# Optimization experiments

Hardware: AMD Instinct MI355X
Metric: run time of the kernel (lower is better)

Reference implementation:

```python
import jax, jax.numpy as jnp
import numpy as np

B, T, C = 2, 2048, 1024
N_HEAD = 16
HEAD_DIM = C // N_HEAD


def setup_inputs() -> dict:
    key = jax.random.key(0)
    k1, k2, k3 = jax.random.split(key, 3)
    x = jax.random.normal(k1, (B, T, C), dtype=jnp.float32)
    w_qkv = jax.random.normal(k2, (C, 3 * C), dtype=jnp.float32) * (C ** -0.5)
    w_proj = jax.random.normal(k3, (C, C), dtype=jnp.float32) * (C ** -0.5)
    b_proj = jnp.zeros((C,), dtype=jnp.float32)
    return {"x": x, "w_qkv": w_qkv, "w_proj": w_proj, "b_proj": b_proj}


def reference(x, w_qkv, w_proj, b_proj):
    Bx, Tx, Cx = x.shape
    # qkv projection: [B,T,3C] -> split into q,k,v each [B,H,T,D]
    qkv = x @ w_qkv  # [B,T,3C]
    qkv = qkv.reshape(Bx, Tx, 3, N_HEAD, HEAD_DIM)
    q = qkv[:, :, 0].transpose(0, 2, 1, 3)  # [B,H,T,D]
    k = qkv[:, :, 1].transpose(0, 2, 1, 3)
    v = qkv[:, :, 2].transpose(0, 2, 1, 3)
    scale = 1.0 / np.sqrt(HEAD_DIM).astype(np.float32)
    att = jnp.einsum('bhtd,bhsd->bhts', q, k) * scale  # [B,H,T,T]
    causal = jnp.tril(jnp.ones((Tx, Tx), dtype=bool))
    att = jnp.where(causal[None, None], att, -jnp.inf)
    att = jax.nn.softmax(att, axis=-1)
    # dropout p=0.0 -> identity (eval-mode math)
    y = jnp.einsum('bhts,bhsd->bhtd', att, v)  # [B,H,T,D]
    y = y.transpose(0, 2, 1, 3).reshape(Bx, Tx, Cx)
    return y @ w_proj + b_proj
```

## Files before the change

### kernel.cpp

```cpp
#include <hip/hip_runtime.h>

typedef __bf16 bf16x8 __attribute__((ext_vector_type(8)));
typedef float f32x4 __attribute__((ext_vector_type(4)));
typedef unsigned short u16;
typedef unsigned int u32;
typedef u32 u32x4 __attribute__((ext_vector_type(4)));
typedef u16 u16x8 __attribute__((ext_vector_type(8)));

#define B_ 2
#define T_ 2048
#define C_ 1024
#define H_ 16
#define D_ 64
#define QSCALE 0.18033688011112042f

__device__ __forceinline__ u16 f2bf(float f) {
    u32 u = __builtin_bit_cast(u32, f);
    u += 0x7fffu + ((u >> 16) & 1u);
    return (u16)(u >> 16);
}

__device__ __forceinline__ f32x4 mfma16(bf16x8 a, bf16x8 b, f32x4 c) {
    return __builtin_amdgcn_mfma_f32_16x16x32_bf16(a, b, c, 0, 0, 0);
}

__device__ __forceinline__ void gll16(const u16* g, u16* l) {
    __builtin_amdgcn_global_load_lds((const __attribute__((address_space(1))) unsigned int*)g,
                                     (__attribute__((address_space(3))) unsigned int*)l,
                                     16, 0, 0);
}

__global__ __launch_bounds__(256) void prep_kernel(const float* __restrict__ x,
                                                   const float* __restrict__ w_qkv,
                                                   const float* __restrict__ w_proj,
                                                   u16* __restrict__ x_bf,
                                                   u16* __restrict__ wqkv_t,
                                                   u16* __restrict__ wproj_t) {
    __shared__ float tile[64][65];
    int bid = blockIdx.x;
    int t = threadIdx.x;
    if (bid < 1024) {
        int base = bid * 4096 + t * 4;
#pragma unroll
        for (int it = 0; it < 4; ++it) {
            int i = base + it * 1024;
            float4 v = *(const float4*)(x + i);
            x_bf[i + 0] = f2bf(v.x);
            x_bf[i + 1] = f2bf(v.y);
            x_bf[i + 2] = f2bf(v.z);
            x_bf[i + 3] = f2bf(v.w);
        }
        return;
    }
    const float* in;
    u16* out;
    int N, tidx;
    if (bid < 1792) { in = w_qkv; out = wqkv_t; N = 3 * C_; tidx = bid - 1024; }
    else            { in = w_proj; out = wproj_t; N = C_;  tidx = bid - 1792; }
    int ntiles = N / 64;
    int n0 = (tidx % ntiles) * 64, k0 = (tidx / ntiles) * 64;
    int c = t & 63, r0 = t >> 6;
    for (int i = 0; i < 16; ++i) {
        int r = r0 * 16 + i;
        tile[r][c] = in[(size_t)(k0 + r) * N + n0 + c];
    }
    __syncthreads();
    for (int i = 0; i < 16; ++i) {
        int rn = r0 * 16 + i;
        out[(size_t)(n0 + rn) * C_ + k0 + c] = f2bf(tile[c][rn]);
    }
}

__global__ __launch_bounds__(256) void qkv_gemm(const u16* __restrict__ x_bf,
                                                const u16* __restrict__ wqkv_t,
                                                u16* __restrict__ Qo, u16* __restrict__ Ko,
                                                u16* __restrict__ Vto) {
    __shared__ __align__(16) u16 smem[16384];
    const int K = 1024;
    int bid = blockIdx.x;
    bool qk = (bid < 512);
    const u16 *A, *Bt;
    int m0, n0;
    if (qk) {
        A = x_bf; Bt = wqkv_t;
        n0 = (bid & 15) * 128; m0 = (bid >> 4) * 128;
    } else {
        int vb = bid - 512;
        A = wqkv_t + 2048 * 1024; Bt = x_bf;
        n0 = (vb & 31) * 128; m0 = (vb >> 5) * 128;
    }
    int t = threadIdx.x;
    int wave = t >> 6, lane = t & 63, lr = lane & 15, quad = lane >> 4;
    int wm = (wave >> 1) * 64, wn = (wave & 1) * 64;

    int srow = lane >> 2;
    int sgl = (lane & 3) ^ ((srow >> 1) & 3);
    int swz = (quad ^ ((lr >> 1) & 3)) * 8;

    f32x4 acc[4][4];
    for (int i = 0; i < 4; ++i)
        for (int j = 0; j < 4; ++j) acc[i][j] = (f32x4){0.f, 0.f, 0.f, 0.f};

    auto stage = [&](int b, int kb) {
        u16* As = smem + b * 4096;
        u16* Bs = smem + 8192 + b * 4096;
        for (int i = 0; i < 2; ++i) {
            int c = wave * 2 + i;
            int row = c * 16 + srow;
            gll16(&A[(size_t)(m0 + row) * K + kb + sgl * 8], &As[c * 512]);
            gll16(&Bt[(size_t)(n0 + row) * K + kb + sgl * 8], &Bs[c * 512]);
        }
    };

    stage(0, 0);
    for (int kt = 0; kt < 32; ++kt) {
        int buf = kt & 1;
        __syncthreads();
        if (kt < 31) stage(buf ^ 1, (kt + 1) * 32);
        const u16* As = smem + buf * 4096;
        const u16* Bs = smem + 8192 + buf * 4096;
        bf16x8 af[4], bfr[4];
        for (int mt = 0; mt < 4; ++mt)
            af[mt] = *(const bf16x8*)&As[(wm + mt * 16 + lr) * 32 + swz];
        for (int nt = 0; nt < 4; ++nt)
            bfr[nt] = *(const bf16x8*)&Bs[(wn + nt * 16 + lr) * 32 + swz];
        for (int mt = 0; mt < 4; ++mt)
            for (int nt = 0; nt < 4; ++nt) acc[mt][nt] = mfma16(af[mt], bfr[nt], acc[mt][nt]);
    }

    __syncthreads();
    u16* eb = smem + wave * 1152;
    int row = lane >> 2;
    int cb = (lane & 3) * 16;
    if (qk) {
        int colg = n0 + wn;
        int part = colg >> 10;
        int h = (colg & 1023) >> 6;
        float sc = (part == 0) ? QSCALE : 1.0f;
        u16* outb = (part == 0) ? Qo : Ko;
#pragma unroll
        for (int p = 0; p < 4; ++p) {
            asm volatile("" ::: "memory");
#pragma unroll
            for (int nt = 0; nt < 4; ++nt)
#pragma unroll
                for (int r = 0; r < 4; ++r)
                    eb[(quad * 4 + r) * 72 + nt * 16 + lr] = f2bf(acc[p][nt][r] * sc);
            asm volatile("" ::: "memory");
            u16x8 va = *(const u16x8*)(eb + row * 72 + cb);
            u16x8 vb = *(const u16x8*)(eb + row * 72 + cb + 8);
            asm volatile("" ::: "memory");
            int rowg = m0 + wm + p * 16 + row;
            int bb = rowg >> 11, tt = rowg & 2047;
            int bh = bb * H_ + h;
            u32* dst = (u32*)(outb + ((size_t)(bh * T_ + tt)) * D_ + cb);
            *(u32x4*)dst = __builtin_bit_cast(u32x4, va);
            *(u32x4*)(dst + 4) = __builtin_bit_cast(u32x4, vb);
        }
    } else {
#pragma unroll
        for (int p = 0; p < 4; ++p) {
            asm volatile("" ::: "memory");
#pragma unroll
            for (int nt = 0; nt < 4; ++nt)
#pragma unroll
                for (int r = 0; r < 4; ++r)
                    eb[(quad * 4 + r) * 72 + nt * 16 + lr] = f2bf(acc[p][nt][r]);
            asm volatile("" ::: "memory");
            u16x8 va = *(const u16x8*)(eb + row * 72 + cb);
            u16x8 vb = *(const u16x8*)(eb + row * 72 + cb + 8);
            asm volatile("" ::: "memory");
            int rowg = m0 + wm + p * 16 + row;
            int h = rowg >> 6, d = rowg & 63;
            int tg = n0 + wn + cb;
            int bb = tg >> 11, tt = tg & 2047;
            u32* dst = (u32*)(Vto + (((size_t)(bb * H_ + h)) * D_ + d) * T_ + tt);
            *(u32x4*)dst = __builtin_bit_cast(u32x4, va);
            *(u32x4*)(dst + 4) = __builtin_bit_cast(u32x4, vb);
        }
    }
}

__global__ __launch_bounds__(256) void gemm64_proj(const u16* __restrict__ A,
                                                   const u16* __restrict__ Bt,
                                                   float* __restrict__ Cout,
                                                   const float* __restrict__ bias,
                                                   int M, int N, int K) {
    __shared__ __align__(16) u16 smem[12288];
    int m0 = blockIdx.y * 128, n0 = blockIdx.x * 64;
    int t = threadIdx.x;
    int wave = t >> 6, lane = t & 63, lr = lane & 15, quad = lane >> 4;
    int srow = lane >> 2;
    int sgl = (lane & 3) ^ ((srow >> 1) & 3);
    int swz = (quad ^ ((lr >> 1) & 3)) * 8;

    f32x4 acc[2][4];
#pragma unroll
    for (int i = 0; i < 2; ++i)
#pragma unroll
        for (int j = 0; j < 4; ++j) acc[i][j] = (f32x4){0.f, 0.f, 0.f, 0.f};

    auto stage = [&](int b, int kb) {
        u16* As = smem + b * 4096;
        u16* Bs = smem + 8192 + b * 2048;
#pragma unroll
        for (int i = 0; i < 2; ++i) {
            int c = wave * 2 + i;
            int row = c * 16 + srow;
            gll16(&A[(size_t)(m0 + row) * K + kb + sgl * 8], &As[c * 512]);
        }
        {
            int row = wave * 16 + srow;
            gll16(&Bt[(size_t)(n0 + row) * K + kb + sgl * 8], &Bs[wave * 512]);
        }
    };

    int niter = K / 32;
    stage(0, 0);
    for (int kt = 0; kt < niter; ++kt) {
        int buf = kt & 1;
        __syncthreads();
        if (kt < niter - 1) stage(buf ^ 1, (kt + 1) * 32);
        const u16* As = smem + buf * 4096;
        const u16* Bs = smem + 8192 + buf * 2048;
        bf16x8 af[2], bfr[4];
#pragma unroll
        for (int mt = 0; mt < 2; ++mt)
            af[mt] = *(const bf16x8*)&As[(wave * 32 + mt * 16 + lr) * 32 + swz];
#pragma unroll
        for (int nt = 0; nt < 4; ++nt)
            bfr[nt] = *(const bf16x8*)&Bs[(nt * 16 + lr) * 32 + swz];
#pragma unroll
        for (int mt = 0; mt < 2; ++mt)
#pragma unroll
            for (int nt = 0; nt < 4; ++nt) acc[mt][nt] = mfma16(af[mt], bfr[nt], acc[mt][nt]);
    }

#pragma unroll
    for (int mt = 0; mt < 2; ++mt)
#pragma unroll
        for (int nt = 0; nt < 4; ++nt)
#pragma unroll
            for (int r = 0; r < 4; ++r) {
                int rowg = m0 + wave * 32 + mt * 16 + quad * 4 + r;
                int col = n0 + nt * 16 + lr;
                Cout[(size_t)rowg * N + col] = acc[mt][nt][r] + bias[col];
            }
}

__global__ __launch_bounds__(256, 4) void attn_kernel(const u16* __restrict__ Q,
                                                      const u16* __restrict__ Kb,
                                                      const u16* __restrict__ Vt,
                                                      u16* __restrict__ Y) {
    __shared__ __align__(16) u16 Kls[2][64 * 64];
    __shared__ __align__(16) u16 Vls[2][64 * 64];
    __shared__ __align__(16) u32 Pls[4][512];
    int qt = 31 - (blockIdx.x >> 5);
    int bh = blockIdx.x & 31;
    int t = threadIdx.x, wave = t >> 6, lane = t & 63, lr = lane & 15, quad = lane >> 4;

    const u16* kbase = Kb + (size_t)bh * (T_ * D_);
    const u16* vbase = Vt + (size_t)bh * (D_ * T_);
    const u16* Qg = Q + ((size_t)bh * T_ + qt * 64 + wave * 16 + lr) * D_;
    bf16x8 qfl = *(const bf16x8*)(Qg + quad * 8);
    bf16x8 qfh = *(const bf16x8*)(Qg + 32 + quad * 8);

    float lsum = 0.f;
    f32x4 o[4];
#pragma unroll
    for (int dt = 0; dt < 4; ++dt) o[dt] = (f32x4){0.f, 0.f, 0.f, 0.f};

    int srow = lane >> 3;
    int sgl = (lane & 7) ^ srow;
    int swz1 = (quad ^ (lr & 7)) * 8;
    int swz2 = ((quad + 4) ^ (lr & 7)) * 8;
    u32* pw = &Pls[wave][0];
    int pwbase = lr * 32 + (quad & 1) * 2;
    int rg1 = (quad ^ (lr & 7)) << 2;
    int rg2 = ((quad + 4) ^ (lr & 7)) << 2;

    for (int i = 0; i < 2; ++i) {
        int c = wave * 2 + i;
        int row = c * 8 + srow;
        gll16(kbase + (size_t)row * D_ + sgl * 8, &Kls[0][c * 512]);
        gll16(vbase + (size_t)row * T_ + sgl * 8, &Vls[0][c * 512]);
    }

    for (int kt = 0; kt <= qt; ++kt) {
        int buf = kt & 1;
        __syncthreads();
        if (kt < qt) {
            int nk = kt + 1;
            for (int i = 0; i < 2; ++i) {
                int c = wave * 2 + i;
                int row = c * 8 + srow;
                gll16(kbase + (size_t)(nk * 64 + row) * D_ + sgl * 8, &Kls[buf ^ 1][c * 512]);
                gll16(vbase + (size_t)row * T_ + nk * 64 + sgl * 8, &Vls[buf ^ 1][c * 512]);
            }
        }
        bf16x8 kf0[4], kf1[4], vf0[4], vf1[4];
#pragma unroll
        for (int st = 0; st < 4; ++st) {
            const u16* kp = &Kls[buf][(st * 16 + lr) * 64];
            kf0[st] = *(const bf16x8*)(kp + swz1);
            kf1[st] = *(const bf16x8*)(kp + swz2);
            const u16* vp = &Vls[buf][(st * 16 + lr) * 64];
            vf0[st] = *(const bf16x8*)(vp + swz1);
            vf1[st] = *(const bf16x8*)(vp + swz2);
        }
        f32x4 s[4];
#pragma unroll
        for (int st = 0; st < 4; ++st) {
            s[st] = mfma16(kf0[st], qfl, (f32x4){0.f, 0.f, 0.f, 0.f});
            s[st] = mfma16(kf1[st], qfh, s[st]);
        }
        if (kt == qt) {
            int qloc = wave * 16 + lr;
#pragma unroll
            for (int st = 0; st < 4; ++st)
#pragma unroll
                for (int r = 0; r < 4; ++r) {
                    if (st * 16 + quad * 4 + r > qloc) s[st][r] = -__builtin_inff();
                }
        }
        float sum = 0.f;
#pragma unroll
        for (int st = 0; st < 4; ++st)
#pragma unroll
            for (int r = 0; r < 4; ++r) {
                float p = __builtin_amdgcn_exp2f(s[st][r]);
                s[st][r] = p;
                sum += p;
            }
        sum += __shfl_xor(sum, 16);
        sum += __shfl_xor(sum, 32);
        lsum += sum;
        asm volatile("" ::: "memory");
#pragma unroll
        for (int st = 0; st < 4; ++st)
#pragma unroll
            for (int rp = 0; rp < 2; ++rp) {
                u32 lo = f2bf(s[st][2 * rp]);
                u32 hi = f2bf(s[st][2 * rp + 1]);
                pw[pwbase + (((st * 2 + (quad >> 1)) ^ (lr & 7)) << 2) + rp] = lo | (hi << 16);
            }
        asm volatile("" ::: "memory");
        const u32* prow = &pw[lr * 32];
        u32x4 plo = *(const u32x4*)(prow + rg1);
        u32x4 phi = *(const u32x4*)(prow + rg2);
        asm volatile("" ::: "memory");
        bf16x8 pfl = __builtin_bit_cast(bf16x8, plo);
        bf16x8 pfh = __builtin_bit_cast(bf16x8, phi);
#pragma unroll
        for (int dt = 0; dt < 4; ++dt) {
            o[dt] = mfma16(vf0[dt], pfl, o[dt]);
            o[dt] = mfma16(vf1[dt], pfh, o[dt]);
        }
    }

    int b = bh >> 4, h = bh & 15;
    float inv = 1.0f / lsum;
    asm volatile("" ::: "memory");
#pragma unroll
    for (int dt = 0; dt < 4; ++dt)
#pragma unroll
        for (int rp = 0; rp < 2; ++rp) {
            u32 lo = f2bf(o[dt][2 * rp] * inv);
            u32 hi = f2bf(o[dt][2 * rp + 1] * inv);
            pw[pwbase + (((dt * 2 + (quad >> 1)) ^ (lr & 7)) << 2) + rp] = lo | (hi << 16);
        }
    asm volatile("" ::: "memory");
    {
        int query = lane >> 2, wsel = lane & 3;
        const u32* prow = &pw[query * 32];
        u32x4 w0 = *(const u32x4*)(prow + (((wsel * 2) ^ (query & 7)) << 2));
        u32x4 w1 = *(const u32x4*)(prow + (((wsel * 2 + 1) ^ (query & 7)) << 2));
        u32* dst = (u32*)(Y + ((size_t)(b * T_ + qt * 64 + wave * 16 + query)) * C_ + h * 64 + wsel * 16);
        *(u32x4*)dst = w0;
        *(u32x4*)(dst + 4) = w1;
    }
}

extern "C" void kernel_launch(void* const* d_in, const int* in_sizes, int n_in,
                              void* d_out, int out_size, void* d_ws, size_t ws_size,
                              hipStream_t stream) {
    const float* x      = (const float*)d_in[0];
    const float* w_qkv  = (const float*)d_in[1];
    const float* w_proj = (const float*)d_in[2];
    const float* b_proj = (const float*)d_in[3];
    float* out = (float*)d_out;

    char* ws = (char*)d_ws;
    u16* x_bf    = (u16*)(ws + 0);
    u16* wqkv_t  = (u16*)(ws + 8388608);
    u16* wproj_t = (u16*)(ws + 14680064);
    u16* q_bf    = (u16*)(ws + 16777216);
    u16* k_bf    = (u16*)(ws + 25165824);
    u16* vt_bf   = (u16*)(ws + 33554432);
    u16* y_bf    = (u16*)(ws + 41943040);

    const int M = B_ * T_;

    prep_kernel<<<2048, 256, 0, stream>>>(x, w_qkv, w_proj, x_bf, wqkv_t, wproj_t);

    qkv_gemm<<<768, 256, 0, stream>>>(x_bf, wqkv_t, q_bf, k_bf, vt_bf);

    attn_kernel<<<32 * (T_ / 64), 256, 0, stream>>>(q_bf, k_bf, vt_bf, y_bf);

    gemm64_proj<<<dim3(C_ / 64, M / 128), 256, 0, stream>>>(
        y_bf, wproj_t, out, b_proj, M, C_, C_);
}
```

Measured before the change: 173.4 us.

## Process 128-query tiles per attention block to reuse K/V loads

Each attention block now handles 128 queries (two 16-row groups per wave) instead of 64, so every K/V tile staged in LDS is used by twice as many queries and global K/V traffic is halved. The grid shrinks from 1024 to 512 blocks, launch bounds drop to 2 blocks per CU, and the P staging buffer doubles. The trade-offs are higher register pressure, fewer blocks for load balancing under the causal mask, and wasted fully masked work in the diagonal tiles.

New measurement: 181.0 us. 4.4% more time.

```diff
diff --git a/kernel.cpp b/kernel.cpp
--- a/kernel.cpp
+++ b/kernel.cpp
@@ -248,33 +248,39 @@
             }
 }
 
-__global__ __launch_bounds__(256, 4) void attn_kernel(const u16* __restrict__ Q,
+__global__ __launch_bounds__(256, 2) void attn_kernel(const u16* __restrict__ Q,
                                                       const u16* __restrict__ Kb,
                                                       const u16* __restrict__ Vt,
                                                       u16* __restrict__ Y) {
     __shared__ __align__(16) u16 Kls[2][64 * 64];
     __shared__ __align__(16) u16 Vls[2][64 * 64];
-    __shared__ __align__(16) u32 Pls[4][512];
-    int qt = 31 - (blockIdx.x >> 5);
-    int bh = blockIdx.x & 31;
+    __shared__ __align__(16) u32 Pls[4][2][512];
+    int bid = blockIdx.x;
+    int qt = 15 - (bid >> 5);
+    int bh = bid & 31;
     int t = threadIdx.x, wave = t >> 6, lane = t & 63, lr = lane & 15, quad = lane >> 4;
 
     const u16* kbase = Kb + (size_t)bh * (T_ * D_);
     const u16* vbase = Vt + (size_t)bh * (D_ * T_);
-    const u16* Qg = Q + ((size_t)bh * T_ + qt * 64 + wave * 16 + lr) * D_;
-    bf16x8 qfl = *(const bf16x8*)(Qg + quad * 8);
-    bf16x8 qfh = *(const bf16x8*)(Qg + 32 + quad * 8);
-
-    float lsum = 0.f;
-    f32x4 o[4];
-#pragma unroll
-    for (int dt = 0; dt < 4; ++dt) o[dt] = (f32x4){0.f, 0.f, 0.f, 0.f};
+    bf16x8 qf[2][2];
+#pragma unroll
+    for (int g = 0; g < 2; ++g) {
+        const u16* Qg = Q + ((size_t)bh * T_ + qt * 128 + wave * 32 + g * 16 + lr) * D_;
+        qf[g][0] = *(const bf16x8*)(Qg + quad * 8);
+        qf[g][1] = *(const bf16x8*)(Qg + 32 + quad * 8);
+    }
+
+    float lsum[2] = {0.f, 0.f};
+    f32x4 o[2][4];
+#pragma unroll
+    for (int g = 0; g < 2; ++g)
+#pragma unroll
+        for (int dt = 0; dt < 4; ++dt) o[g][dt] = (f32x4){0.f, 0.f, 0.f, 0.f};
 
     int srow = lane >> 3;
     int sgl = (lane & 7) ^ srow;
     int swz1 = (quad ^ (lr & 7)) * 8;
     int swz2 = ((quad + 4) ^ (lr & 7)) * 8;
-    u32* pw = &Pls[wave][0];
     int pwbase = lr * 32 + (quad & 1) * 2;
     int rg1 = (quad ^ (lr & 7)) << 2;
     int rg2 = ((quad + 4) ^ (lr & 7)) << 2;
@@ -286,10 +292,11 @@
         gll16(vbase + (size_t)row * T_ + sgl * 8, &Vls[0][c * 512]);
     }
 
-    for (int kt = 0; kt <= qt; ++kt) {
+    int ktmax = 2 * qt + 1;
+    for (int kt = 0; kt <= ktmax; ++kt) {
         int buf = kt & 1;
         __syncthreads();
-        if (kt < qt) {
+        if (kt < ktmax) {
             int nk = kt + 1;
             for (int i = 0; i < 2; ++i) {
                 int c = wave * 2 + i;
@@ -308,74 +315,91 @@
             vf0[st] = *(const bf16x8*)(vp + swz1);
             vf1[st] = *(const bf16x8*)(vp + swz2);
         }
-        f32x4 s[4];
-#pragma unroll
-        for (int st = 0; st < 4; ++st) {
-            s[st] = mfma16(kf0[st], qfl, (f32x4){0.f, 0.f, 0.f, 0.f});
-            s[st] = mfma16(kf1[st], qfh, s[st]);
-        }
-        if (kt == qt) {
-            int qloc = wave * 16 + lr;
+        f32x4 s[2][4];
+#pragma unroll
+        for (int g = 0; g < 2; ++g)
+#pragma unroll
+            for (int st = 0; st < 4; ++st) {
+                s[g][st] = mfma16(kf0[st], qf[g][0], (f32x4){0.f, 0.f, 0.f, 0.f});
+                s[g][st] = mfma16(kf1[st], qf[g][1], s[g][st]);
+            }
+        if (kt >= ktmax - 1) {
+#pragma unroll
+            for (int g = 0; g < 2; ++g) {
+                int qloc = qt * 128 - kt * 64 + wave * 32 + g * 16 + lr;
+#pragma unroll
+                for (int st = 0; st < 4; ++st)
+#pragma unroll
+                    for (int r = 0; r < 4; ++r) {
+                        if (st * 16 + quad * 4 + r > qloc) s[g][st][r] = -__builtin_inff();
+                    }
+            }
+        }
+#pragma unroll
+        for (int g = 0; g < 2; ++g) {
+            float sum = 0.f;
 #pragma unroll
             for (int st = 0; st < 4; ++st)
 #pragma unroll
                 for (int r = 0; r < 4; ++r) {
-                    if (st * 16 + quad * 4 + r > qloc) s[st][r] = -__builtin_inff();
+                    float p = __builtin_amdgcn_exp2f(s[g][st][r]);
+                    s[g][st][r] = p;
+                    sum += p;
                 }
-        }
-        float sum = 0.f;
-#pragma unroll
-        for (int st = 0; st < 4; ++st)
-#pragma unroll
-            for (int r = 0; r < 4; ++r) {
-                float p = __builtin_amdgcn_exp2f(s[st][r]);
-                s[st][r] = p;
-                sum += p;
-            }
-        sum += __shfl_xor(sum, 16);
-        sum += __shfl_xor(sum, 32);
-        lsum += sum;
+            sum += __shfl_xor(sum, 16);
+            sum += __shfl_xor(sum, 32);
+            lsum[g] += sum;
+        }
         asm volatile("" ::: "memory");
 #pragma unroll
-        for (int st = 0; st < 4; ++st)
+        for (int g = 0; g < 2; ++g) {
+            u32* pw = &Pls[wave][g][0];
+#pragma unroll
+            for (int st = 0; st < 4; ++st)
+#pragma unroll
+                for (int rp = 0; rp < 2; ++rp) {
+                    u32 lo = f2bf(s[g][st][2 * rp]);
+                    u32 hi = f2bf(s[g][st][2 * rp + 1]);
+                    pw[pwbase + (((st * 2 + (quad >> 1)) ^ (lr & 7)) << 2) + rp] = lo | (hi << 16);
+                }
+        }
+        asm volatile("" ::: "memory");
+#pragma unroll
+        for (int g = 0; g < 2; ++g) {
+            const u32* prow = &Pls[wave][g][lr * 32];
+            u32x4 plo = *(const u32x4*)(prow + rg1);
+            u32x4 phi = *(const u32x4*)(prow + rg2);
+            asm volatile("" ::: "memory");
+            bf16x8 pfl = __builtin_bit_cast(bf16x8, plo);
+            bf16x8 pfh = __builtin_bit_cast(bf16x8, phi);
+#pragma unroll
+            for (int dt = 0; dt < 4; ++dt) {
+                o[g][dt] = mfma16(vf0[dt], pfl, o[g][dt]);
+                o[g][dt] = mfma16(vf1[dt], pfh, o[g][dt]);
+            }
+        }
+    }
+
+    int b = bh >> 4, h = bh & 15;
+#pragma unroll
+    for (int g = 0; g < 2; ++g) {
+        float inv = 1.0f / lsum[g];
+        u32* pw = &Pls[wave][g][0];
+        asm volatile("" ::: "memory");
+#pragma unroll
+        for (int dt = 0; dt < 4; ++dt)
 #pragma unroll
             for (int rp = 0; rp < 2; ++rp) {
-                u32 lo = f2bf(s[st][2 * rp]);
-                u32 hi = f2bf(s[st][2 * rp + 1]);
-                pw[pwbase + (((st * 2 + (quad >> 1)) ^ (lr & 7)) << 2) + rp] = lo | (hi << 16);
+                u32 lo = f2bf(o[g][dt][2 * rp] * inv);
+                u32 hi = f2bf(o[g][dt][2 * rp + 1] * inv);
+                pw[pwbase + (((dt * 2 + (quad >> 1)) ^ (lr & 7)) << 2) + rp] = lo | (hi << 16);
             }
         asm volatile("" ::: "memory");
-        const u32* prow = &pw[lr * 32];
-        u32x4 plo = *(const u32x4*)(prow + rg1);
-        u32x4 phi = *(const u32x4*)(prow + rg2);
-        asm volatile("" ::: "memory");
-        bf16x8 pfl = __builtin_bit_cast(bf16x8, plo);
-        bf16x8 pfh = __builtin_bit_cast(bf16x8, phi);
-#pragma unroll
-        for (int dt = 0; dt < 4; ++dt) {
-            o[dt] = mfma16(vf0[dt], pfl, o[dt]);
-            o[dt] = mfma16(vf1[dt], pfh, o[dt]);
-        }
-    }
-
-    int b = bh >> 4, h = bh & 15;
-    float inv = 1.0f / lsum;
-    asm volatile("" ::: "memory");
-#pragma unroll
-    for (int dt = 0; dt < 4; ++dt)
-#pragma unroll
-        for (int rp = 0; rp < 2; ++rp) {
-            u32 lo = f2bf(o[dt][2 * rp] * inv);
-            u32 hi = f2bf(o[dt][2 * rp + 1] * inv);
-            pw[pwbase + (((dt * 2 + (quad >> 1)) ^ (lr & 7)) << 2) + rp] = lo | (hi << 16);
-        }
-    asm volatile("" ::: "memory");
-    {
         int query = lane >> 2, wsel = lane & 3;
         const u32* prow = &pw[query * 32];
         u32x4 w0 = *(const u32x4*)(prow + (((wsel * 2) ^ (query & 7)) << 2));
         u32x4 w1 = *(const u32x4*)(prow + (((wsel * 2 + 1) ^ (query & 7)) << 2));
-        u32* dst = (u32*)(Y + ((size_t)(b * T_ + qt * 64 + wave * 16 + query)) * C_ + h * 64 + wsel * 16);
+        u32* dst = (u32*)(Y + ((size_t)(b * T_ + qt * 128 + wave * 32 + g * 16 + query)) * C_ + h * 64 + wsel * 16);
         *(u32x4*)dst = w0;
         *(u32x4*)(dst + 4) = w1;
     }
@@ -405,7 +429,7 @@
 
     qkv_gemm<<<768, 256, 0, stream>>>(x_bf, wqkv_t, q_bf, k_bf, vt_bf);
 
-    attn_kernel<<<32 * (T_ / 64), 256, 0, stream>>>(q_bf, k_bf, vt_bf, y_bf);
+    attn_kernel<<<512, 256, 0, stream>>>(q_bf, k_bf, vt_bf, y_bf);
 
     gemm64_proj<<<dim3(C_ / 64, M / 128), 256, 0, stream>>>(
         y_bf, wproj_t, out, b_proj, M, C_, C_);
```
